# Kernel tuning notes

Measured on AMD Instinct MI355X. Metric: run time of the kernel, lower is better.

## Reference

```python
import jax, jax.numpy as jnp
import numpy as np

K, D = 4096, 256
BETA, DECAY, EPS = 0.25, 0.99, 1e-05
B = 32768


def setup_inputs() -> dict:
    key = jax.random.key(0)
    k1, k2, k3, k4 = jax.random.split(key, 4)
    return {
        "z_e": jax.random.normal(k1, (B, D), dtype=jnp.float32),
        "codebook": jax.random.normal(k2, (K, D), dtype=jnp.float32),
        "ema_cluster_size": jax.random.uniform(k3, (K,), dtype=jnp.float32),
        "ema_weight": jax.random.normal(k4, (K, D), dtype=jnp.float32),
    }


def reference(z_e, codebook, ema_cluster_size, ema_weight):
    z_e = z_e.astype(jnp.float32)
    # squared L2 distances: ||z||^2 - 2 z.C^T + ||C||^2  (chunking in torch is
    # purely a memory optimization; math is identical)
    e_norm = jnp.sum(z_e * z_e, axis=1, keepdims=True)            # [B,1]
    c_norm = jnp.sum(codebook * codebook, axis=1)                  # [K]
    dists = e_norm - 2.0 * (z_e @ codebook.T) + c_norm[None, :]    # [B,K]
    idx = jnp.argmin(dists, axis=1)                                # [B] int

    z_q = codebook[idx]                                            # [B,d] gather

    # EMA codebook update (no_grad in torch)
    counts = jnp.zeros((K,), jnp.float32).at[idx].add(1.0)         # bincount
    new_cluster = ema_cluster_size * DECAY + counts * (1.0 - DECAY)
    dw = jnp.zeros((K, D), jnp.float32).at[idx].add(z_e)           # index_add_
    new_ema_weight = ema_weight * DECAY + dw * (1.0 - DECAY)
    n = jnp.sum(new_cluster)
    cluster_size = (new_cluster + EPS) / (n + K * EPS) * n
    new_codebook = new_ema_weight / cluster_size[:, None]

    z_q_ste = z_e + jax.lax.stop_gradient(z_q - z_e)
    commit = BETA * jnp.mean((z_e - z_q) ** 2)
    return (z_q_ste, idx, commit, new_codebook, new_cluster, new_ema_weight)
```

## Files before the change

kernel.cpp:

```cpp
#include <hip/hip_runtime.h>

#define KC 4096
#define DD 256
#define BB 32768
#define P_BETA 0.25f
#define P_DECAY 0.99f
#define P_EPS 1e-5f
#define TAU 0.5f
#define CHUNK 32

typedef __attribute__((ext_vector_type(8))) short bf16x8;
typedef __attribute__((ext_vector_type(4))) float f32x4;

static __device__ __forceinline__ unsigned short f2bf(float f) {
    unsigned int u = __float_as_uint(f);
    unsigned int r = (u + 0x7fffu + ((u >> 16) & 1u)) >> 16;
    return (unsigned short)r;
}
static __device__ __forceinline__ void gload_lds16(const void* g, void* s) {
    __builtin_amdgcn_global_load_lds(
        (const __attribute__((address_space(1))) unsigned int*)g,
        (__attribute__((address_space(3))) unsigned int*)s, 16, 0, 0);
}

#define ZBLK (BB * DD / 4 / 256)
#define CBLK (KC * DD / 4 / 256)
__global__ __launch_bounds__(256) void convert_all_kernel(
    const float* __restrict__ z, const float* __restrict__ cb,
    unsigned short* __restrict__ zb, unsigned short* __restrict__ cbb,
    float* __restrict__ cn, int* __restrict__ cnt) {
    const int b = blockIdx.x;
    if (b < ZBLK) {
        int t = b * 256 + threadIdx.x;
        float4 v = ((const float4*)z)[t];
        *(ushort4*)&zb[(size_t)t * 4] =
            make_ushort4(f2bf(v.x), f2bf(v.y), f2bf(v.z), f2bf(v.w));
    } else if (b < ZBLK + CBLK) {
        int t = (b - ZBLK) * 256 + threadIdx.x;
        int lane = threadIdx.x & 63;
        int row = (b - ZBLK) * 4 + (threadIdx.x >> 6);
        float4 v = ((const float4*)cb)[t];
        *(ushort4*)&cbb[(size_t)t * 4] =
            make_ushort4(f2bf(v.x), f2bf(v.y), f2bf(v.z), f2bf(v.w));
        float s = v.x * v.x + v.y * v.y + v.z * v.z + v.w * v.w;
#pragma unroll
        for (int m = 32; m; m >>= 1) s += __shfl_xor(s, m);
        if (lane == 0) cn[row] = s;
    } else {
        int4* p = (int4*)cnt;
        int4 zv = make_int4(0, 0, 0, 0);
#pragma unroll
        for (int j = 0; j < 4; ++j) p[threadIdx.x * 4 + j] = zv;
    }
}

__global__ __launch_bounds__(256, 2) void
mfma_argmin_kernel(const unsigned short* __restrict__ zb,
                   const unsigned short* __restrict__ cbb,
                   const float* __restrict__ cn,
                   float4* __restrict__ cand) {
    __shared__ unsigned short As[128 * 256];
    __shared__ unsigned short Bs[128 * 64];

    const int tid = threadIdx.x;
    const int l = tid & 63, w = tid >> 6;
    const int xcd = blockIdx.x & 7;
    const int half = xcd >> 2;
    const int rb = (blockIdx.x >> 3) * 4 + (xcd & 3);
    const int row0 = rb * 128;
    const int col0 = half * 2048;
    const int wm = w & 1, wn = w >> 1;
    const int m_off = wm * 64, n_off = wn * 64;
    const int lm = l & 15, lq = l >> 4;

    {
        const int lrow = w * 2 + (l >> 5);
        const int coff = ((l & 31) ^ lrow) * 8;
#pragma unroll
        for (int i = 0; i < 16; ++i) {
            gload_lds16(zb + (size_t)(row0 + i * 8 + lrow) * DD + coff,
                        &As[(i * 8 + w * 2) * 256]);
        }
    }

    const int srow = l >> 3;
    const int scol = ((l & 7) ^ srow) * 8;
    const int g0 = w * 4;

    float best[16];
    int bidx[16];
#pragma unroll
    for (int s = 0; s < 16; ++s) { best[s] = 3.4e38f; bidx[s] = 0; }

    for (int kc = 0; kc < 2048; kc += 128) {
        f32x4 acc[4][4];
#pragma unroll
        for (int a = 0; a < 4; ++a)
#pragma unroll
            for (int b = 0; b < 4; ++b) acc[a][b] = (f32x4){0.f, 0.f, 0.f, 0.f};

        for (int dc = 0; dc < 4; ++dc) {
#pragma unroll
            for (int j = 0; j < 4; ++j) {
                const int g = g0 + j;
                const int br = col0 + kc + g * 8 + srow;
                gload_lds16(cbb + (size_t)br * DD + dc * 64 + scol, &Bs[g * 512]);
            }
            __syncthreads();
#pragma unroll
            for (int ks = 0; ks < 2; ++ks) {
                bf16x8 af[4], bfr[4];
                const int cbi = dc * 8 + ks * 4 + lq;
#pragma unroll
                for (int tm = 0; tm < 4; ++tm) {
                    int r = m_off + tm * 16 + lm;
                    af[tm] = *(const bf16x8*)&As[r * 256 + ((cbi ^ (r & 7)) * 8)];
                }
#pragma unroll
                for (int tn = 0; tn < 4; ++tn) {
                    int r = n_off + tn * 16 + lm;
                    bfr[tn] = *(const bf16x8*)&Bs[r * 64 + (((ks * 4 + lq) ^ (r & 7)) * 8)];
                }
#pragma unroll
                for (int tm = 0; tm < 4; ++tm)
#pragma unroll
                    for (int tn = 0; tn < 4; ++tn)
                        acc[tm][tn] = __builtin_amdgcn_mfma_f32_16x16x32_bf16(
                            af[tm], bfr[tn], acc[tm][tn], 0, 0, 0);
            }
            __syncthreads();
        }
#pragma unroll
        for (int tn = 0; tn < 4; ++tn) {
            const int col = col0 + kc + n_off + tn * 16 + lm;
            const float cnv = cn[col];
#pragma unroll
            for (int tm = 0; tm < 4; ++tm)
#pragma unroll
                for (int r = 0; r < 4; ++r) {
                    float dist = fmaf(-2.0f, acc[tm][tn][r], cnv);
                    int s = tm * 4 + r;
                    if (dist < best[s]) { best[s] = dist; bidx[s] = col; }
                }
        }
    }

    float v2[16];
    int i2[16];
#pragma unroll
    for (int s = 0; s < 16; ++s) { v2[s] = 3.4e38f; i2[s] = 0x7fffffff; }
#pragma unroll
    for (int m = 1; m < 16; m <<= 1) {
#pragma unroll
        for (int s = 0; s < 16; ++s) {
            float w1 = __shfl_xor(best[s], m); int j1 = __shfl_xor(bidx[s], m);
            float w2 = __shfl_xor(v2[s], m);   int j2 = __shfl_xor(i2[s], m);
            bool b = (w1 < best[s]) || (w1 == best[s] && j1 < bidx[s]);
            if (b) {
                bool c = (best[s] < w2) || (best[s] == w2 && bidx[s] < j2);
                v2[s] = c ? best[s] : w2; i2[s] = c ? bidx[s] : j2;
                best[s] = w1; bidx[s] = j1;
            } else {
                bool c = (w1 < v2[s]) || (w1 == v2[s] && j1 < i2[s]);
                v2[s] = c ? w1 : v2[s]; i2[s] = c ? j1 : i2[s];
            }
        }
    }

    float4* red = (float4*)As;
    if (lm == 0) {
#pragma unroll
        for (int tm = 0; tm < 4; ++tm)
#pragma unroll
            for (int r = 0; r < 4; ++r) {
                int s = tm * 4 + r;
                int row_local = m_off + tm * 16 + lq * 4 + r;
                red[wn * 128 + row_local] =
                    make_float4(best[s], __int_as_float(bidx[s]), v2[s], __int_as_float(i2[s]));
            }
    }
    __syncthreads();
    if (tid < 128) {
        float4 a = red[tid], b = red[128 + tid];
        float av1 = a.x, av2 = a.z; int ai1 = __float_as_int(a.y), ai2 = __float_as_int(a.w);
        float bv1 = b.x, bv2 = b.z; int bi1 = __float_as_int(b.y), bi2 = __float_as_int(b.w);
        float v1o, v2o; int i1o, i2o;
        bool bb = (bv1 < av1) || (bv1 == av1 && bi1 < ai1);
        if (bb) {
            v1o = bv1; i1o = bi1;
            bool c = (av1 < bv2) || (av1 == bv2 && ai1 < bi2);
            v2o = c ? av1 : bv2; i2o = c ? ai1 : bi2;
        } else {
            v1o = av1; i1o = ai1;
            bool c = (bv1 < av2) || (bv1 == av2 && bi1 < ai2);
            v2o = c ? bv1 : av2; i2o = c ? bi1 : ai2;
        }
        cand[(size_t)half * BB + row0 + tid] =
            make_float4(v1o, __int_as_float(i1o), v2o, __int_as_float(i2o));
    }
}

__global__ __launch_bounds__(256) void merge_refine_kernel(
    const float4* __restrict__ cand, const float* __restrict__ z,
    const float* __restrict__ cb, const float* __restrict__ cn,
    int* __restrict__ idx_i, float* __restrict__ idx_f,
    int* __restrict__ cnt, float* __restrict__ dw) {
    int i = blockIdx.x * 256 + threadIdx.x;
    {
        float4 zv4 = make_float4(0.f, 0.f, 0.f, 0.f);
        float4* dp = (float4*)dw;
        int base = i * 8;
#pragma unroll
        for (int j = 0; j < 8; ++j) dp[base + j] = zv4;
    }
    float4 a = cand[i], b = cand[(size_t)BB + i];
    float av1 = a.x, av2 = a.z; int ai1 = __float_as_int(a.y), ai2 = __float_as_int(a.w);
    float bv1 = b.x, bv2 = b.z; int bi1 = __float_as_int(b.y), bi2 = __float_as_int(b.w);
    float v1o, v2o; int i1o, i2o;
    bool bb = (bv1 < av1) || (bv1 == av1 && bi1 < ai1);
    if (bb) {
        v1o = bv1; i1o = bi1;
        bool c = (av1 < bv2) || (av1 == bv2 && ai1 < bi2);
        v2o = c ? av1 : bv2; i2o = c ? ai1 : bi2;
    } else {
        v1o = av1; i1o = ai1;
        bool c = (bv1 < av2) || (bv1 == av2 && bi1 < ai2);
        v2o = c ? bv1 : av2; i2o = c ? bi1 : ai2;
    }
    int kb = i1o;
    if (v2o - v1o < TAU) {
        const float4* zr = (const float4*)(z + (size_t)i * DD);
        const float4* c1 = (const float4*)(cb + (size_t)i1o * DD);
        const float4* c2 = (const float4*)(cb + (size_t)i2o * DD);
        float s1x = 0, s1y = 0, s1z = 0, s1w = 0;
        float s2x = 0, s2y = 0, s2z = 0, s2w = 0;
        for (int j = 0; j < 64; ++j) {
            float4 zv = zr[j], p = c1[j], q = c2[j];
            s1x = fmaf(zv.x, p.x, s1x); s1y = fmaf(zv.y, p.y, s1y);
            s1z = fmaf(zv.z, p.z, s1z); s1w = fmaf(zv.w, p.w, s1w);
            s2x = fmaf(zv.x, q.x, s2x); s2y = fmaf(zv.y, q.y, s2y);
            s2z = fmaf(zv.z, q.z, s2z); s2w = fmaf(zv.w, q.w, s2w);
        }
        float d1 = cn[i1o] - 2.f * ((s1x + s1y) + (s1z + s1w));
        float d2 = cn[i2o] - 2.f * ((s2x + s2y) + (s2z + s2w));
        if (d2 < d1 || (d2 == d1 && i2o < i1o)) kb = i2o;
    }
    idx_i[i] = kb;
    idx_f[i] = (float)kb;
    atomicAdd(&cnt[kb], 1);
}

__global__ __launch_bounds__(256) void prefix_kernel(const int* __restrict__ cnt,
                                                     int* __restrict__ cursor) {
    __shared__ int ls[257];
    const int t = threadIdx.x;
    int local[16];
    int s = 0;
#pragma unroll
    for (int j = 0; j < 16; ++j) { local[j] = s; s += cnt[t * 16 + j]; }
    ls[t + 1] = s;
    __syncthreads();
    if (t == 0) {
        ls[0] = 0;
        for (int j = 1; j <= 256; ++j) ls[j] += ls[j - 1];
    }
    __syncthreads();
    int off = ls[t];
#pragma unroll
    for (int j = 0; j < 16; ++j) cursor[t * 16 + j] = off + local[j];
}

__global__ __launch_bounds__(256) void zq_commit_scatter_kernel(
    const float* __restrict__ z, const float* __restrict__ cb,
    const int* __restrict__ idx_i, float* __restrict__ zq,
    float* __restrict__ commit_parts, int* __restrict__ cursor,
    int* __restrict__ row_of) {
    const int w = threadIdx.x >> 6, l = threadIdx.x & 63;
    const int i = blockIdx.x * 4 + w;
    const int k = idx_i[i];
    float4 zv = ((const float4*)z)[(size_t)i * 64 + l];
    float4 cv = ((const float4*)cb)[(size_t)k * 64 + l];
    ((float4*)zq)[(size_t)i * 64 + l] = cv;
    float dx = zv.x - cv.x, dy = zv.y - cv.y, dz = zv.z - cv.z, dq = zv.w - cv.w;
    float s = dx * dx + dy * dy + dz * dz + dq * dq;
#pragma unroll
    for (int m = 32; m; m >>= 1) s += __shfl_xor(s, m);
    __shared__ float ls[4];
    if (l == 0) {
        ls[w] = s;
        int pos = atomicAdd(&cursor[k], 1);
        row_of[pos] = i | (k << 16);
    }
    __syncthreads();
    if (threadIdx.x == 0) commit_parts[blockIdx.x] = ls[0] + ls[1] + ls[2] + ls[3];
}

__global__ __launch_bounds__(256) void bucket_cluster_kernel(
    const float* __restrict__ z, const int* __restrict__ row_of,
    float* __restrict__ dw, const float* __restrict__ ema_cs,
    const int* __restrict__ cnt, const float* __restrict__ commit_parts,
    float* __restrict__ out_cluster, float* __restrict__ n_ws,
    float* __restrict__ out_commit) {
    const int t = threadIdx.x;
    if (blockIdx.x == BB / CHUNK) {
        float cs = 0.f;
        for (int j = t; j < BB / 4; j += 256) cs += commit_parts[j];
        float ns = 0.f;
        for (int j = t; j < KC; j += 256) {
            float nc = ema_cs[j] * P_DECAY + (float)cnt[j] * (1.0f - P_DECAY);
            out_cluster[j] = nc;
            ns += nc;
        }
#pragma unroll
        for (int m = 32; m; m >>= 1) { cs += __shfl_xor(cs, m); ns += __shfl_xor(ns, m); }
        __shared__ float lc[4], ln[4];
        if ((t & 63) == 0) { lc[t >> 6] = cs; ln[t >> 6] = ns; }
        __syncthreads();
        if (t == 0) {
            *out_commit = P_BETA * (lc[0] + lc[1] + lc[2] + lc[3]) / (float)((size_t)BB * DD);
            *n_ws = ln[0] + ln[1] + ln[2] + ln[3];
        }
        return;
    }
    __shared__ int pk[CHUNK];
    const int p0 = blockIdx.x * CHUNK;
    if (t < CHUNK) pk[t] = row_of[p0 + t];
    __syncthreads();
    float acc = 0.f;
    int kprev = pk[0] >> 16;
#pragma unroll 4
    for (int j = 0; j < CHUNK; ++j) {
        int p = pk[j];
        int r = p & 0xffff, k = p >> 16;
        if (k != kprev) {
            atomicAdd(&dw[(size_t)kprev * DD + t], acc);
            acc = 0.f;
            kprev = k;
        }
        acc += z[(size_t)r * DD + t];
    }
    atomicAdd(&dw[(size_t)kprev * DD + t], acc);
}

__global__ __launch_bounds__(256) void finalize_kernel(const float* __restrict__ ema_w,
                                                       const float* __restrict__ dw,
                                                       const float* __restrict__ out_cluster,
                                                       const float* __restrict__ n_ws,
                                                       float* __restrict__ out_ema_w,
                                                       float* __restrict__ out_codebook) {
    const size_t id = (size_t)blockIdx.x * 256 + threadIdx.x;
    const int k = (int)(id >> 8);
    const float n = *n_ws;
    float nw = ema_w[id] * P_DECAY + dw[id] * (1.0f - P_DECAY);
    out_ema_w[id] = nw;
    float cl = out_cluster[k];
    float csz = (cl + P_EPS) / (n + (float)KC * P_EPS) * n;
    out_codebook[id] = nw / csz;
}

extern "C" void kernel_launch(void* const* d_in, const int* in_sizes, int n_in,
                              void* d_out, int out_size, void* d_ws, size_t ws_size,
                              hipStream_t stream) {
    const float* z      = (const float*)d_in[0];
    const float* cb     = (const float*)d_in[1];
    const float* ema_cs = (const float*)d_in[2];
    const float* ema_w  = (const float*)d_in[3];

    float4* cand = (float4*)d_ws;
    unsigned short* zb = (unsigned short*)(cand + 2 * (size_t)BB);
    unsigned short* cbb = zb + (size_t)BB * DD;
    float* dw = (float*)(cbb + (size_t)KC * DD);
    float* c_norm = dw + (size_t)KC * DD;
    int* idx_i = (int*)(c_norm + KC);
    int* cnt = idx_i + BB;
    int* cursor = cnt + KC;
    int* row_of = cursor + KC;
    float* commit_parts = (float*)(row_of + BB);
    float* n_ws = commit_parts + BB / 4;

    float* out        = (float*)d_out;
    float* o_zq       = out;
    float* o_idx      = o_zq + (size_t)BB * DD;
    float* o_commit   = o_idx + BB;
    float* o_codebook = o_commit + 1;
    float* o_cluster  = o_codebook + (size_t)KC * DD;
    float* o_emaw     = o_cluster + KC;

    convert_all_kernel<<<ZBLK + CBLK + 1, 256, 0, stream>>>(z, cb, zb, cbb, c_norm, cnt);
    mfma_argmin_kernel<<<(BB / 128) * 2, 256, 0, stream>>>(zb, cbb, c_norm, cand);
    merge_refine_kernel<<<BB / 256, 256, 0, stream>>>(cand, z, cb, c_norm, idx_i,
                                                      o_idx, cnt, dw);
    prefix_kernel<<<1, 256, 0, stream>>>(cnt, cursor);
    zq_commit_scatter_kernel<<<BB / 4, 256, 0, stream>>>(z, cb, idx_i, o_zq,
                                                         commit_parts, cursor, row_of);
    bucket_cluster_kernel<<<BB / CHUNK + 1, 256, 0, stream>>>(z, row_of, dw, ema_cs,
                                                              cnt, commit_parts,
                                                              o_cluster, n_ws, o_commit);
    finalize_kernel<<<(KC * DD) / 256, 256, 0, stream>>>(ema_w, dw, o_cluster, n_ws,
                                                         o_emaw, o_codebook);
    (void)in_sizes; (void)n_in; (void)out_size; (void)ws_size;
}
```

Before: 235.7 us.

## Double-buffer codebook tiles and keep half of the A tile in registers

The codebook tile in LDS is now double-buffered, so the next chunk's global-to-LDS load is issued before the current chunk's MFMAs run. This removes one barrier per step. To free LDS for the second buffer, only the first half of each z row is kept in LDS and the second half is loaded once into registers (16 bf16x8 per lane). The cost is much higher register pressure, which could spill or reduce occupancy under launch_bounds(256,2).

```diff
diff --git a/kernel.cpp b/kernel.cpp
--- a/kernel.cpp
+++ b/kernel.cpp
@@ -59,8 +59,8 @@
                    const unsigned short* __restrict__ cbb,
                    const float* __restrict__ cn,
                    float4* __restrict__ cand) {
-    __shared__ unsigned short As[128 * 256];
-    __shared__ unsigned short Bs[128 * 64];
+    __shared__ unsigned short As[128 * 128];
+    __shared__ unsigned short Bs[2][128 * 64];
 
     const int tid = threadIdx.x;
     const int l = tid & 63, w = tid >> 6;
@@ -74,24 +74,48 @@
     const int lm = l & 15, lq = l >> 4;
 
     {
-        const int lrow = w * 2 + (l >> 5);
-        const int coff = ((l & 31) ^ lrow) * 8;
-#pragma unroll
-        for (int i = 0; i < 16; ++i) {
-            gload_lds16(zb + (size_t)(row0 + i * 8 + lrow) * DD + coff,
-                        &As[(i * 8 + w * 2) * 256]);
+        const int lr = (l >> 4);
+        const int c = l & 15;
+#pragma unroll
+        for (int i = 0; i < 8; ++i) {
+            const int r = i * 16 + w * 4 + lr;
+            gload_lds16(zb + (size_t)(row0 + r) * DD + ((c ^ (r & 7)) * 8),
+                        &As[(i * 16 + w * 4) * 128]);
         }
     }
 
     const int srow = l >> 3;
     const int scol = ((l & 7) ^ srow) * 8;
     const int g0 = w * 4;
+    auto stageB = [&](int buf, int s) {
+        const int kcn = (s >> 2) * 128;
+        const int dcn = (s & 3) * 64;
+#pragma unroll
+        for (int j = 0; j < 4; ++j) {
+            const int g = g0 + j;
+            const int br = col0 + kcn + g * 8 + srow;
+            gload_lds16(cbb + (size_t)br * DD + dcn + scol, &Bs[buf][g * 512]);
+        }
+    };
+    stageB(0, 0);
+
+    bf16x8 afr[4][4];
+#pragma unroll
+    for (int tm = 0; tm < 4; ++tm) {
+        const size_t grow = (size_t)(row0 + m_off + tm * 16 + lm) * DD;
+#pragma unroll
+        for (int t = 0; t < 4; ++t)
+            afr[tm][t] = *(const bf16x8*)&zb[grow + 128 + t * 32 + lq * 8];
+    }
+
+    __syncthreads();
 
     float best[16];
     int bidx[16];
 #pragma unroll
     for (int s = 0; s < 16; ++s) { best[s] = 3.4e38f; bidx[s] = 0; }
 
+    int cur = 0;
     for (int kc = 0; kc < 2048; kc += 128) {
         f32x4 acc[4][4];
 #pragma unroll
@@ -99,27 +123,28 @@
 #pragma unroll
             for (int b = 0; b < 4; ++b) acc[a][b] = (f32x4){0.f, 0.f, 0.f, 0.f};
 
+#pragma unroll
         for (int dc = 0; dc < 4; ++dc) {
-#pragma unroll
-            for (int j = 0; j < 4; ++j) {
-                const int g = g0 + j;
-                const int br = col0 + kc + g * 8 + srow;
-                gload_lds16(cbb + (size_t)br * DD + dc * 64 + scol, &Bs[g * 512]);
-            }
-            __syncthreads();
+            const int ns = (kc >> 7) * 4 + dc + 1;
+            if (ns < 64) stageB(cur ^ 1, ns);
 #pragma unroll
             for (int ks = 0; ks < 2; ++ks) {
                 bf16x8 af[4], bfr[4];
-                const int cbi = dc * 8 + ks * 4 + lq;
-#pragma unroll
-                for (int tm = 0; tm < 4; ++tm) {
-                    int r = m_off + tm * 16 + lm;
-                    af[tm] = *(const bf16x8*)&As[r * 256 + ((cbi ^ (r & 7)) * 8)];
-                }
 #pragma unroll
                 for (int tn = 0; tn < 4; ++tn) {
                     int r = n_off + tn * 16 + lm;
-                    bfr[tn] = *(const bf16x8*)&Bs[r * 64 + (((ks * 4 + lq) ^ (r & 7)) * 8)];
+                    bfr[tn] = *(const bf16x8*)&Bs[cur][r * 64 + (((ks * 4 + lq) ^ (r & 7)) * 8)];
+                }
+                if (dc < 2) {
+                    const int cbi = dc * 8 + ks * 4 + lq;
+#pragma unroll
+                    for (int tm = 0; tm < 4; ++tm) {
+                        int r = m_off + tm * 16 + lm;
+                        af[tm] = *(const bf16x8*)&As[r * 128 + ((cbi ^ (r & 7)) * 8)];
+                    }
+                } else {
+#pragma unroll
+                    for (int tm = 0; tm < 4; ++tm) af[tm] = afr[tm][(dc - 2) * 2 + ks];
                 }
 #pragma unroll
                 for (int tm = 0; tm < 4; ++tm)
@@ -129,7 +154,9 @@
                             af[tm], bfr[tn], acc[tm][tn], 0, 0, 0);
             }
             __syncthreads();
-        }
+            cur ^= 1;
+        }
+
 #pragma unroll
         for (int tn = 0; tn < 4; ++tn) {
             const int col = col0 + kc + n_off + tn * 16 + lm;
```

Result: slower. 255.6 us (+8.5%).

## Fuse per-code bucket gather into finalize and drop the atomic dw accumulation

Applied to the files above, without the earlier changes.

Replaces the chunked bucket kernel, which used atomicAdd into a zeroed dw buffer, plus the separate finalize kernel with one kernel per codebook entry. Each block sums its own bucket of rows using cursor and cnt, then writes the new ema_weight and codebook rows directly. The cluster-size and n computation moves into the single-block prefix kernel. This removes the dw zeroing, the global atomics and one full kernel plus its buffer round trip, at the cost of load imbalance when bucket sizes are uneven and a serial dependent loop over each bucket.

```diff
diff --git a/kernel.cpp b/kernel.cpp
--- a/kernel.cpp
+++ b/kernel.cpp
@@ -7,7 +7,6 @@
 #define P_DECAY 0.99f
 #define P_EPS 1e-5f
 #define TAU 0.5f
-#define CHUNK 32
 
 typedef __attribute__((ext_vector_type(8))) short bf16x8;
 typedef __attribute__((ext_vector_type(4))) float f32x4;
@@ -204,15 +203,8 @@
     const float4* __restrict__ cand, const float* __restrict__ z,
     const float* __restrict__ cb, const float* __restrict__ cn,
     int* __restrict__ idx_i, float* __restrict__ idx_f,
-    int* __restrict__ cnt, float* __restrict__ dw) {
+    int* __restrict__ cnt) {
     int i = blockIdx.x * 256 + threadIdx.x;
-    {
-        float4 zv4 = make_float4(0.f, 0.f, 0.f, 0.f);
-        float4* dp = (float4*)dw;
-        int base = i * 8;
-#pragma unroll
-        for (int j = 0; j < 8; ++j) dp[base + j] = zv4;
-    }
     float4 a = cand[i], b = cand[(size_t)BB + i];
     float av1 = a.x, av2 = a.z; int ai1 = __float_as_int(a.y), ai2 = __float_as_int(a.w);
     float bv1 = b.x, bv2 = b.z; int bi1 = __float_as_int(b.y), bi2 = __float_as_int(b.w);
@@ -250,19 +242,33 @@
     atomicAdd(&cnt[kb], 1);
 }
 
-__global__ __launch_bounds__(256) void prefix_kernel(const int* __restrict__ cnt,
-                                                     int* __restrict__ cursor) {
+__global__ __launch_bounds__(256) void prefix_kernel(
+    const int* __restrict__ cnt, int* __restrict__ cursor,
+    const float* __restrict__ ema_cs, float* __restrict__ out_cluster,
+    float* __restrict__ n_ws) {
     __shared__ int ls[257];
+    __shared__ float lns[4];
     const int t = threadIdx.x;
     int local[16];
     int s = 0;
-#pragma unroll
-    for (int j = 0; j < 16; ++j) { local[j] = s; s += cnt[t * 16 + j]; }
+    float ns = 0.f;
+#pragma unroll
+    for (int j = 0; j < 16; ++j) {
+        int c = cnt[t * 16 + j];
+        local[j] = s; s += c;
+        float nc = ema_cs[t * 16 + j] * P_DECAY + (float)c * (1.0f - P_DECAY);
+        out_cluster[t * 16 + j] = nc;
+        ns += nc;
+    }
     ls[t + 1] = s;
+#pragma unroll
+    for (int m = 32; m; m >>= 1) ns += __shfl_xor(ns, m);
+    if ((t & 63) == 0) lns[t >> 6] = ns;
     __syncthreads();
     if (t == 0) {
         ls[0] = 0;
         for (int j = 1; j <= 256; ++j) ls[j] += ls[j - 1];
+        *n_ws = lns[0] + lns[1] + lns[2] + lns[3];
     }
     __syncthreads();
     int off = ls[t];
@@ -295,63 +301,37 @@
     if (threadIdx.x == 0) commit_parts[blockIdx.x] = ls[0] + ls[1] + ls[2] + ls[3];
 }
 
-__global__ __launch_bounds__(256) void bucket_cluster_kernel(
+__global__ __launch_bounds__(256) void gather_finalize_kernel(
     const float* __restrict__ z, const int* __restrict__ row_of,
-    float* __restrict__ dw, const float* __restrict__ ema_cs,
-    const int* __restrict__ cnt, const float* __restrict__ commit_parts,
-    float* __restrict__ out_cluster, float* __restrict__ n_ws,
+    const int* __restrict__ cursor, const int* __restrict__ cnt,
+    const float* __restrict__ ema_w, const float* __restrict__ out_cluster,
+    const float* __restrict__ n_ws, const float* __restrict__ commit_parts,
+    float* __restrict__ out_ema_w, float* __restrict__ out_codebook,
     float* __restrict__ out_commit) {
     const int t = threadIdx.x;
-    if (blockIdx.x == BB / CHUNK) {
+    const int k = blockIdx.x;
+    if (k == KC) {
         float cs = 0.f;
         for (int j = t; j < BB / 4; j += 256) cs += commit_parts[j];
-        float ns = 0.f;
-        for (int j = t; j < KC; j += 256) {
-            float nc = ema_cs[j] * P_DECAY + (float)cnt[j] * (1.0f - P_DECAY);
-            out_cluster[j] = nc;
-            ns += nc;
-        }
-#pragma unroll
-        for (int m = 32; m; m >>= 1) { cs += __shfl_xor(cs, m); ns += __shfl_xor(ns, m); }
-        __shared__ float lc[4], ln[4];
-        if ((t & 63) == 0) { lc[t >> 6] = cs; ln[t >> 6] = ns; }
+#pragma unroll
+        for (int m = 32; m; m >>= 1) cs += __shfl_xor(cs, m);
+        __shared__ float lc[4];
+        if ((t & 63) == 0) lc[t >> 6] = cs;
         __syncthreads();
-        if (t == 0) {
+        if (t == 0)
             *out_commit = P_BETA * (lc[0] + lc[1] + lc[2] + lc[3]) / (float)((size_t)BB * DD);
-            *n_ws = ln[0] + ln[1] + ln[2] + ln[3];
-        }
         return;
     }
-    __shared__ int pk[CHUNK];
-    const int p0 = blockIdx.x * CHUNK;
-    if (t < CHUNK) pk[t] = row_of[p0 + t];
-    __syncthreads();
+    const int e = cursor[k];
+    const int c = cnt[k];
     float acc = 0.f;
-    int kprev = pk[0] >> 16;
-#pragma unroll 4
-    for (int j = 0; j < CHUNK; ++j) {
-        int p = pk[j];
-        int r = p & 0xffff, k = p >> 16;
-        if (k != kprev) {
-            atomicAdd(&dw[(size_t)kprev * DD + t], acc);
-            acc = 0.f;
-            kprev = k;
-        }
+    for (int j = e - c; j < e; ++j) {
+        int r = row_of[j] & 0xffff;
         acc += z[(size_t)r * DD + t];
     }
-    atomicAdd(&dw[(size_t)kprev * DD + t], acc);
-}
-
-__global__ __launch_bounds__(256) void finalize_kernel(const float* __restrict__ ema_w,
-                                                       const float* __restrict__ dw,
-                                                       const float* __restrict__ out_cluster,
-                                                       const float* __restrict__ n_ws,
-                                                       float* __restrict__ out_ema_w,
-                                                       float* __restrict__ out_codebook) {
-    const size_t id = (size_t)blockIdx.x * 256 + threadIdx.x;
-    const int k = (int)(id >> 8);
     const float n = *n_ws;
-    float nw = ema_w[id] * P_DECAY + dw[id] * (1.0f - P_DECAY);
+    const size_t id = (size_t)k * DD + t;
+    float nw = ema_w[id] * P_DECAY + acc * (1.0f - P_DECAY);
     out_ema_w[id] = nw;
     float cl = out_cluster[k];
     float csz = (cl + P_EPS) / (n + (float)KC * P_EPS) * n;
@@ -369,8 +349,7 @@
     float4* cand = (float4*)d_ws;
     unsigned short* zb = (unsigned short*)(cand + 2 * (size_t)BB);
     unsigned short* cbb = zb + (size_t)BB * DD;
-    float* dw = (float*)(cbb + (size_t)KC * DD);
-    float* c_norm = dw + (size_t)KC * DD;
+    float* c_norm = (float*)(cbb + (size_t)KC * DD);
     int* idx_i = (int*)(c_norm + KC);
     int* cnt = idx_i + BB;
     int* cursor = cnt + KC;
@@ -389,14 +368,13 @@
     convert_all_kernel<<<ZBLK + CBLK + 1, 256, 0, stream>>>(z, cb, zb, cbb, c_norm, cnt);
     mfma_argmin_kernel<<<(BB / 128) * 2, 256, 0, stream>>>(zb, cbb, c_norm, cand);
     merge_refine_kernel<<<BB / 256, 256, 0, stream>>>(cand, z, cb, c_norm, idx_i,
-                                                      o_idx, cnt, dw);
-    prefix_kernel<<<1, 256, 0, stream>>>(cnt, cursor);
+                                                      o_idx, cnt);
+    prefix_kernel<<<1, 256, 0, stream>>>(cnt, cursor, ema_cs, o_cluster, n_ws);
     zq_commit_scatter_kernel<<<BB / 4, 256, 0, stream>>>(z, cb, idx_i, o_zq,
                                                          commit_parts, cursor, row_of);
-    bucket_cluster_kernel<<<BB / CHUNK + 1, 256, 0, stream>>>(z, row_of, dw, ema_cs,
-                                                              cnt, commit_parts,
-                                                              o_cluster, n_ws, o_commit);
-    finalize_kernel<<<(KC * DD) / 256, 256, 0, stream>>>(ema_w, dw, o_cluster, n_ws,
-                                                         o_emaw, o_codebook);
+    gather_finalize_kernel<<<KC + 1, 256, 0, stream>>>(z, row_of, cursor, cnt,
+                                                       ema_w, o_cluster, n_ws,
+                                                       commit_parts, o_emaw,
+                                                       o_codebook, o_commit);
     (void)in_sizes; (void)n_in; (void)out_size; (void)ws_size;
 }
```

New measurement: 434.4 us. 1.84x slower.
